# Kernel tuning notes

Hardware: AMD Instinct MI355X
Metric: run time of the kernel (lower is better)

The kernel has to match this reference:

```python
import jax, jax.numpy as jnp
import numpy as np

N = 8192
D_IN = 512
HID = 1024
EMB = 64
N_EFF = 2
N_CLASSES = 16
MARGIN = 0.01


def setup_inputs() -> dict:
    key = jax.random.key(0)
    ks = jax.random.split(key, 10)
    data = jax.random.normal(ks[0], (N, D_IN), dtype=jnp.float32)
    labels = jax.random.randint(ks[1], (N,), 0, N_CLASSES).astype(jnp.float32)
    x = jnp.concatenate([labels[:, None], data], axis=1)  # [N, 1+D_IN]

    def lin(k, fan_in, fan_out):
        return jax.random.normal(k, (fan_in, fan_out), dtype=jnp.float32) / np.sqrt(fan_in)

    return {
        "x": x,
        "W1": lin(ks[2], D_IN, HID), "b1": jnp.zeros((HID,), jnp.float32),
        "W2": lin(ks[3], HID, EMB), "b2": jnp.zeros((EMB,), jnp.float32),
        "W3": lin(ks[4], EMB, HID), "b3": jnp.zeros((HID,), jnp.float32),
        "W4": lin(ks[5], HID, D_IN), "b4": jnp.zeros((D_IN,), jnp.float32),
    }


def reference(x, W1, b1, W2, b2, W3, b3, W4, b4):
    labels = x[:, 0]
    data = x[:, 1:]

    # encoder / decoder (tanh MLP autoencoder)
    embedding = jnp.tanh(data @ W1 + b1) @ W2 + b2          # [N, EMB]
    decoded = jnp.tanh(embedding @ W3 + b3) @ W4 + b4       # [N, D_IN]

    conserved = embedding[:, N_EFF:]                        # [N, C]
    n_conserved = conserved.shape[1]

    # labels.expand + unique(return_inverse) on row-replicated labels is
    # equivalent to comparing the labels directly.
    lbl = labels.astype(jnp.int32)
    Y = lbl[:, None] != lbl[None, :]                        # [N, N] bool

    # D_mean[i,j] = mean_d (c_i - c_j)^2, via Gram-matrix algebra (one pass,
    # no [N,N,C] intermediate).
    sq = jnp.sum(conserved * conserved, axis=1)             # [N]
    gram = conserved @ conserved.T                          # [N, N]
    D_mean = jnp.maximum(sq[:, None] + sq[None, :] - 2.0 * gram, 0.0) / n_conserved

    Yf = Y.astype(D_mean.dtype)
    n_diff = jnp.sum(Yf)
    C_sim = jnp.sum(Yf * D_mean) / (n_diff + 1.0)
    C_diff = jnp.sum((1.0 - Yf) * jnp.maximum(0.0, MARGIN - D_mean)) / (
        (D_mean.shape[0] * D_mean.shape[1] - n_diff) + 1.0)

    return decoded, C_sim, C_diff
```

## Files before the change

### kernel.cpp

```cpp
#include <hip/hip_runtime.h>
#include <stdint.h>

#define NROWS 8192
#define DIN   512
#define HIDN  1024
#define EMBN  64
#define NCONS 62
#define NCLS  16
#define MARGINF 0.01f
#define NREP  16

typedef unsigned short u16;
typedef __attribute__((ext_vector_type(8))) short short8;
typedef __attribute__((ext_vector_type(4))) float floatx4;

__device__ __forceinline__ u16 f32_to_bf16(float f) {
  union { float f; uint32_t u; } x; x.f = f;
  uint32_t u = x.u;
  uint32_t r = (u + 0x7FFFu + ((u >> 16) & 1u)) >> 16;
  return (u16)r;
}

__device__ __forceinline__ float bf16_to_f32(u16 h) {
  union { uint32_t u; float f; } x; x.u = (uint32_t)h << 16;
  return x.f;
}

__device__ __forceinline__ float fast_tanh(float x) {
  float xc = fminf(fmaxf(x, -10.f), 10.f);
  float e = __expf(2.f * xc);
  return (e - 1.f) * __builtin_amdgcn_rcpf(e + 1.f);
}

__device__ __forceinline__ void pack_tile(const float* __restrict__ W,
                                          u16* __restrict__ Wp,
                                          int N, int KU, int t, int lane)
{
  const int r = lane >> 2, slot = lane & 3;
  const int c = slot ^ ((r >> 1) & 3);
  const int nt = t / KU, ku = t - nt * KU;
  const int n = nt * 16 + r;
  const int kb = ku * 32 + c * 8;
  short8 v;
#pragma unroll
  for (int j = 0; j < 8; ++j) v[j] = (short)f32_to_bf16(W[(size_t)(kb + j) * N + n]);
  *(short8*)(Wp + ((size_t)t * 64 + lane) * 8) = v;
}

__global__ __launch_bounds__(256)
void prep_all(const float* __restrict__ x,
              const float* __restrict__ W1, const float* __restrict__ W2,
              const float* __restrict__ W3, const float* __restrict__ W4,
              u16* __restrict__ A0p, u16* __restrict__ W1p,
              u16* __restrict__ W2p, u16* __restrict__ W3p,
              u16* __restrict__ W4p, float* __restrict__ slab,
              int* __restrict__ labels, int* __restrict__ hist32)
{
  __shared__ int hh[NCLS];
  const int b = blockIdx.x;
  const int tid = threadIdx.x;
  const int tl = tid >> 6, lane = tid & 63;
  if (b < 2048) {
    if (b < 32) {
      if (tid < NCLS) hh[tid] = 0;
      const int row = b * 256 + tid;
      const int lab = (int)x[(size_t)row * 513];
      labels[row] = lab;
      __syncthreads();
      atomicAdd(&hh[lab], 1);
      __syncthreads();
      if (tid < NCLS) hist32[b * NCLS + tid] = hh[tid];
    }
    const int t = b * 4 + tl;
    const int rt = t >> 4, ku = t & 15;
    const int r = lane & 15, q = lane >> 4;
    const float* src = x + (size_t)(rt * 16 + r) * 513 + 1 + ku * 32 + q * 8;
    short8 v;
#pragma unroll
    for (int j = 0; j < 8; ++j) v[j] = (short)f32_to_bf16(src[j]);
    *(short8*)(A0p + ((size_t)t * 64 + lane) * 8) = v;
  } else if (b < 2304) {
    pack_tile(W1, W1p, 1024, 16, (b - 2048) * 4 + tl, lane);
  } else if (b < 2336) {
    pack_tile(W2, W2p, 64, 32, (b - 2304) * 4 + tl, lane);
  } else if (b < 2368) {
    pack_tile(W3, W3p, 1024, 2, (b - 2336) * 4 + tl, lane);
  } else if (b < 2624) {
    pack_tile(W4, W4p, 512, 32, (b - 2368) * 4 + tl, lane);
  } else {
    float* dst = slab + (size_t)(b - 2624) * 4096;
    for (int i = tid; i < 4096; i += 256) dst[i] = 0.f;
  }
}

__global__ __launch_bounds__(512, 4)
void fused1234(const u16* __restrict__ A0p, const u16* __restrict__ W1p,
               const float* __restrict__ b1, const u16* __restrict__ W2p,
               const float* __restrict__ b2, const u16* __restrict__ W3p,
               const float* __restrict__ b3, const u16* __restrict__ W4p,
               const float* __restrict__ b4,
               const int* __restrict__ labels, const int* __restrict__ hist32,
               int* __restrict__ offs, int* __restrict__ counts,
               int* __restrict__ idx,
               u16* __restrict__ Ebf, float* __restrict__ sqrow,
               float* __restrict__ vsumR, float* __restrict__ SsumR,
               float* __restrict__ out)
{
  __shared__ u16 uni[16 * 1032];
  __shared__ u16 El[16 * 66];
  __shared__ float lv[NCLS][64];
  __shared__ float lsq[NCLS][64];
  __shared__ int colsum[NCLS], preblk[NCLS], scur[NCLS];

  const int tid = threadIdx.x;

  if (blockIdx.x < 16) {
    const int sb = blockIdx.x;
    if (tid < NCLS) {
      int s = 0, p = 0;
      for (int b2i = 0; b2i < 32; ++b2i) {
        const int h = hist32[b2i * NCLS + tid];
        s += h;
        if (b2i < sb * 2) p += h;
      }
      colsum[tid] = s;
      preblk[tid] = p;
    }
    __syncthreads();
    if (tid < NCLS) {
      int o = 0;
      for (int c = 0; c < tid; ++c) o += colsum[c];
      scur[tid] = o + preblk[tid];
      if (sb == 0) {
        counts[tid] = colsum[tid];
        offs[tid] = o;
        if (tid == NCLS - 1) offs[NCLS] = o + colsum[NCLS - 1];
      }
    }
    __syncthreads();
    {
      const int row = sb * 512 + tid;
      const int p = atomicAdd(&scur[labels[row]], 1);
      idx[p] = row;
    }
    return;
  }

  const int bx = blockIdx.x - 16;
  const int m0 = bx * 16;
  const int rep = blockIdx.x & (NREP - 1);
  const int w = tid >> 6, lane = tid & 63;
  const int quad = lane >> 4, l15 = lane & 15;
  const int lamb = l15 * 4 + (quad ^ ((l15 >> 1) & 3));

  for (int i = tid; i < NCLS * 64; i += 512) {
    ((float*)lv)[i] = 0.f; ((float*)lsq)[i] = 0.f;
  }

  u16* Hc = uni;
  float* Epart = (float*)uni;
  u16* Tl = uni;

  const u16* Wbase = W1p + (size_t)(w * 8) * 16 * 512 + lamb * 8;
  const u16* Abase = A0p + (size_t)(bx * 16) * 512 + lane * 8;

  floatx4 acc1[8];
#pragma unroll
  for (int jj = 0; jj < 8; ++jj) acc1[jj] = (floatx4){0.f, 0.f, 0.f, 0.f};

  short8 bfb[2][8];
  short8 afb[2];
  afb[0] = *(const short8*)(Abase);
#pragma unroll
  for (int jj = 0; jj < 8; ++jj)
    bfb[0][jj] = *(const short8*)(Wbase + (size_t)(jj * 16) * 512);

#pragma unroll
  for (int s = 0; s < 16; ++s) {
    const int cur = s & 1, nxt = cur ^ 1;
    if (s < 15) {
      afb[nxt] = *(const short8*)(Abase + (size_t)(s + 1) * 512);
#pragma unroll
      for (int jj = 0; jj < 8; ++jj)
        bfb[nxt][jj] = *(const short8*)(Wbase + (size_t)(jj * 16 + s + 1) * 512);
    }
#pragma unroll
    for (int jj = 0; jj < 8; ++jj)
      acc1[jj] = __builtin_amdgcn_mfma_f32_16x16x32_bf16(afb[cur], bfb[cur][jj], acc1[jj], 0, 0, 0);
  }

#pragma unroll
  for (int jj = 0; jj < 8; ++jj) {
    const int col = w * 128 + jj * 16 + l15;
    const float bv = b1[col];
#pragma unroll
    for (int r = 0; r < 4; ++r)
      Hc[(quad * 4 + r) * 1032 + col] = f32_to_bf16(fast_tanh(acc1[jj][r] + bv));
  }
  __syncthreads();

  floatx4 acc2[4];
#pragma unroll
  for (int nt = 0; nt < 4; ++nt) acc2[nt] = (floatx4){0.f, 0.f, 0.f, 0.f};

#pragma unroll
  for (int kk = 0; kk < 4; ++kk) {
    const int ku = w * 4 + kk;
    const short8 af = *(const short8*)(Hc + l15 * 1032 + ku * 32 + quad * 8);
#pragma unroll
    for (int nt = 0; nt < 4; ++nt) {
      const short8 bf = *(const short8*)(W2p + (size_t)(nt * 32 + ku) * 512 + lamb * 8);
      acc2[nt] = __builtin_amdgcn_mfma_f32_16x16x32_bf16(af, bf, acc2[nt], 0, 0, 0);
    }
  }
  __syncthreads();

#pragma unroll
  for (int nt = 0; nt < 4; ++nt)
#pragma unroll
    for (int r = 0; r < 4; ++r)
      Epart[((size_t)w * 16 + quad * 4 + r) * 64 + nt * 16 + l15] = acc2[nt][r];
  __syncthreads();

  {
    const float bv2 = b2[lane];
    for (int r = 0; r < 2; ++r) {
      const int row = w * 2 + r;
      const int grow = m0 + row;
      const int c = labels[grow];
      float acc = bv2;
#pragma unroll
      for (int p = 0; p < 8; ++p)
        acc += Epart[((size_t)p * 16 + row) * 64 + lane];
      const u16 h = f32_to_bf16(acc);
      Ebf[(size_t)grow * 64 + lane] = h;
      El[row * 66 + lane] = h;
      float v = bf16_to_f32(h);
      if (lane < 2) v = 0.f;
      const float v2 = v * v;
      atomicAdd(&lv[c][lane], v);
      atomicAdd(&lsq[c][lane], v2);
      float s = v2;
      for (int o = 32; o > 0; o >>= 1) s += __shfl_xor(s, o);
      if (lane == 0) sqrow[grow] = s;
    }
  }
  __syncthreads();

  for (int i = tid; i < NCLS * 64; i += 512) {
    const int c = i >> 6, k = i & 63;
    if (k >= 2) atomicAdd(&vsumR[rep * (NCLS * NCONS) + c * NCONS + k - 2], lv[c][k]);
  }
  if (tid < NCLS) {
    float s = 0.f;
    for (int k = 0; k < 64; ++k) s += lsq[tid][k];
    atomicAdd(&SsumR[rep * NCLS + tid], s);
  }

  floatx4 acc3[8];
#pragma unroll
  for (int jj = 0; jj < 8; ++jj) acc3[jj] = (floatx4){0.f, 0.f, 0.f, 0.f};

#pragma unroll
  for (int kk = 0; kk < 2; ++kk) {
    const short8 af = *(const short8*)(El + l15 * 66 + kk * 32 + quad * 8);
#pragma unroll
    for (int jj = 0; jj < 8; ++jj) {
      const int nt = w * 8 + jj;
      const short8 bf = *(const short8*)(W3p + (size_t)(nt * 2 + kk) * 512 + lamb * 8);
      acc3[jj] = __builtin_amdgcn_mfma_f32_16x16x32_bf16(af, bf, acc3[jj], 0, 0, 0);
    }
  }
#pragma unroll
  for (int jj = 0; jj < 8; ++jj) {
    const int col = w * 128 + jj * 16 + l15;
    const float bv3 = b3[col];
#pragma unroll
    for (int r = 0; r < 4; ++r)
      Tl[(quad * 4 + r) * 1032 + col] = f32_to_bf16(fast_tanh(acc3[jj][r] + bv3));
  }
  __syncthreads();

  const u16* W4base = W4p + (size_t)(w * 4) * 32 * 512 + lamb * 8;

  floatx4 acc4[4];
#pragma unroll
  for (int nt = 0; nt < 4; ++nt) acc4[nt] = (floatx4){0.f, 0.f, 0.f, 0.f};

  short8 b4b[2][4];
  short8 a4b[2];
  a4b[0] = *(const short8*)(Tl + l15 * 1032 + quad * 8);
#pragma unroll
  for (int nt = 0; nt < 4; ++nt)
    b4b[0][nt] = *(const short8*)(W4base + (size_t)(nt * 32) * 512);

#pragma unroll
  for (int ku = 0; ku < 32; ++ku) {
    const int cur = ku & 1, nxt = cur ^ 1;
    if (ku < 31) {
      a4b[nxt] = *(const short8*)(Tl + l15 * 1032 + (ku + 1) * 32 + quad * 8);
#pragma unroll
      for (int nt = 0; nt < 4; ++nt)
        b4b[nxt][nt] = *(const short8*)(W4base + (size_t)(nt * 32 + ku + 1) * 512);
    }
#pragma unroll
    for (int nt = 0; nt < 4; ++nt)
      acc4[nt] = __builtin_amdgcn_mfma_f32_16x16x32_bf16(a4b[cur], b4b[cur][nt], acc4[nt], 0, 0, 0);
  }

#pragma unroll
  for (int nt = 0; nt < 4; ++nt) {
    const int col = w * 64 + nt * 16 + l15;
    const float bv4 = b4[col];
#pragma unroll
    for (int r = 0; r < 4; ++r) {
      const int row = m0 + quad * 4 + r;
      out[(size_t)row * 512 + col] = acc4[nt][r] + bv4;
    }
  }
}

__global__ __launch_bounds__(256)
void pairwise_mfma(const u16* __restrict__ Ebf, const float* __restrict__ sqrow,
                   const int* __restrict__ idx, const int* __restrict__ offs,
                   float* __restrict__ pair_sum)
{
  const int q = blockIdx.x;
  const int cls = q / 21;
  int p = q - cls * 21, ti = 0, cnt = 6;
  while (p >= cnt) { p -= cnt; ++ti; --cnt; }
  const int tj = ti + p;

  const int start = offs[cls];
  const int n = offs[cls + 1] - start;
  if (ti * 128 >= n || tj * 128 >= n) return;

  constexpr int LDA = 66;
  __shared__ u16 Li[128 * LDA];
  __shared__ u16 Lj[128 * LDA];
  __shared__ float sqI[128], sqJ[128];
  __shared__ float red4[4];

  const int tid = threadIdx.x, wave = tid >> 6, lane = tid & 63;
  const int quad = lane >> 4, l15 = lane & 15;

  for (int e = tid; e < 2048; e += 256) {
    const int t = e >> 10;
    const int row = (e >> 3) & 127;
    const int ch = e & 7;
    const int g = (t ? tj : ti) * 128 + row;
    short8 v = (short8)0;
    if (g < n) {
      v = *(const short8*)(Ebf + (size_t)idx[start + g] * EMBN + ch * 8);
      if (ch == 0) { v[0] = 0; v[1] = 0; }
    }
    *(short8*)((t ? Lj : Li) + row * LDA + ch * 8) = v;
  }
  {
    const int t = tid >> 7, row = tid & 127;
    const int g = (t ? tj : ti) * 128 + row;
    (t ? sqJ : sqI)[row] = (g < n) ? sqrow[idx[start + g]] : 0.f;
  }
  __syncthreads();

  const int wm = wave >> 1, wn = wave & 1;

  floatx4 acc[4][4];
#pragma unroll
  for (int i = 0; i < 4; ++i)
#pragma unroll
    for (int j = 0; j < 4; ++j) acc[i][j] = (floatx4){0.f, 0.f, 0.f, 0.f};

#pragma unroll
  for (int ks = 0; ks < 2; ++ks) {
    short8 af[4], bf[4];
#pragma unroll
    for (int i = 0; i < 4; ++i)
      af[i] = *(const short8*)(Li + (wm * 64 + i * 16 + l15) * LDA + ks * 32 + quad * 8);
#pragma unroll
    for (int j = 0; j < 4; ++j)
      bf[j] = *(const short8*)(Lj + (wn * 64 + j * 16 + l15) * LDA + ks * 32 + quad * 8);
#pragma unroll
    for (int i = 0; i < 4; ++i)
#pragma unroll
      for (int j = 0; j < 4; ++j)
        acc[i][j] = __builtin_amdgcn_mfma_f32_16x16x32_bf16(af[i], bf[j], acc[i][j], 0, 0, 0);
  }

  float local = 0.f;
#pragma unroll
  for (int i = 0; i < 4; ++i)
#pragma unroll
    for (int j = 0; j < 4; ++j)
#pragma unroll
      for (int r = 0; r < 4; ++r) {
        const int row = wm * 64 + i * 16 + quad * 4 + r;
        const int col = wn * 64 + j * 16 + l15;
        const int gi = ti * 128 + row, gj = tj * 128 + col;
        if (gi < n && gj < n && gi != gj) {
          const float D = (sqI[row] + sqJ[col] - 2.f * acc[i][j][r]) * (1.f / 62.f);
          local += fmaxf(0.f, MARGINF - D);
        }
      }
  if (ti < tj) local *= 2.f;

  for (int o = 32; o > 0; o >>= 1) local += __shfl_xor(local, o);
  if (lane == 0) red4[wave] = local;
  __syncthreads();
  if (tid == 0)
    atomicAdd(pair_sum, red4[0] + red4[1] + red4[2] + red4[3]);
}

__device__ __forceinline__ double block_reduce_d(double v, double* red, int tid) {
  red[tid] = v;
  __syncthreads();
  for (int st = 128; st > 0; st >>= 1) {
    if (tid < st) red[tid] += red[tid + st];
    __syncthreads();
  }
  const double r = red[0];
  __syncthreads();
  return r;
}

__global__ __launch_bounds__(256)
void finalize(const float* __restrict__ vsumR, const float* __restrict__ SsumR,
              const int* __restrict__ counts, const float* __restrict__ pair_sum,
              float* __restrict__ out2)
{
  const int tid = threadIdx.x;
  __shared__ double red[256];
  __shared__ float vtot[NCLS * NCONS];

  for (int i = tid; i < NCLS * NCONS; i += 256) {
    float s = 0.f;
    for (int r = 0; r < NREP; ++r) s += vsumR[r * (NCLS * NCONS) + i];
    vtot[i] = s;
  }
  __syncthreads();

  double v = 0.0;
  if (tid < NCLS) {
    float Sc = 0.f;
    for (int r = 0; r < NREP; ++r) Sc += SsumR[r * NCLS + tid];
    v = (double)Sc * (double)(NROWS - counts[tid]);
  }
  const double t1 = block_reduce_d(v, red, tid);

  v = 0.0;
  if (tid < NCLS) { const double nc = (double)counts[tid]; v = nc * nc; }
  const double n_same = block_reduce_d(v, red, tid);

  v = 0.0;
  for (int i = tid; i < NCLS * NCONS; i += 256) { const double w = vtot[i]; v += w * w; }
  const double t2 = block_reduce_d(v, red, tid);

  v = 0.0;
  if (tid < NCONS) {
    double Vk = 0.0;
    for (int c = 0; c < NCLS; ++c) Vk += (double)vtot[c * NCONS + tid];
    v = Vk * Vk;
  }
  const double t3 = block_reduce_d(v, red, tid);

  if (tid == 0) {
    const double n_diff = (double)NROWS * (double)NROWS - n_same;
    const double sim = 2.0 * t1 - 2.0 * (t3 - t2);
    const double C_sim = sim / 62.0 / (n_diff + 1.0);
    const double C_diff = ((double)pair_sum[0] + (double)NROWS * (double)MARGINF)
                          / (n_same + 1.0);
    out2[0] = (float)C_sim;
    out2[1] = (float)C_diff;
  }
}

extern "C" void kernel_launch(void* const* d_in, const int* in_sizes, int n_in,
                              void* d_out, int out_size, void* d_ws, size_t ws_size,
                              hipStream_t stream)
{
  const float* x  = (const float*)d_in[0];
  const float* W1 = (const float*)d_in[1];
  const float* b1 = (const float*)d_in[2];
  const float* W2 = (const float*)d_in[3];
  const float* b2 = (const float*)d_in[4];
  const float* W3 = (const float*)d_in[5];
  const float* b3 = (const float*)d_in[6];
  const float* W4 = (const float*)d_in[7];
  const float* b4 = (const float*)d_in[8];
  float* out = (float*)d_out;

  char* ws = (char*)d_ws;
  const size_t KB = 1024, MB = 1ull << 20;
  u16* A0p    = (u16*)(ws + 0);
  u16* W1p    = (u16*)(ws + 8 * MB);
  u16* W2p    = (u16*)(ws + 9 * MB);
  u16* W3p    = (u16*)(ws + 9 * MB + 128 * KB);
  u16* W4p    = (u16*)(ws + 9 * MB + 256 * KB);
  u16* Ebf    = (u16*)(ws + 18 * MB + 256 * KB);
  int* labels = (int*)(ws + 19 * MB + 256 * KB);
  int* idx    = (int*)(ws + 19 * MB + 288 * KB);
  float* sqrow = (float*)(ws + 19 * MB + 320 * KB);
  int* hist32 = (int*)(ws + 19 * MB + 352 * KB);
  float* slab = (float*)(ws + 19 * MB + 384 * KB);
  int*   counts  = (int*)slab;
  int*   offs    = counts + 16;
  float* psum    = slab + 64;
  float* SsumR   = slab + 128;
  float* vsumR   = slab + 512;
  (void)in_sizes; (void)n_in; (void)out_size; (void)ws_size;

  prep_all<<<dim3(2630), dim3(256), 0, stream>>>(x, W1, W2, W3, W4,
                                                 A0p, W1p, W2p, W3p, W4p,
                                                 slab, labels, hist32);
  fused1234<<<dim3(528), dim3(512), 0, stream>>>(A0p, W1p, b1, W2p, b2, W3p, b3,
                                                 W4p, b4,
                                                 labels, hist32, offs, counts, idx,
                                                 Ebf, sqrow, vsumR, SsumR, out);
  pairwise_mfma<<<dim3(336), dim3(256), 0, stream>>>(Ebf, sqrow, idx, offs, psum);
  finalize<<<dim3(1), dim3(256), 0, stream>>>(vsumR, SsumR, counts, psum,
                                              out + (size_t)NROWS * DIN);
}
```

Before: 159.9 us.

## Process 32 rows per block in fused MLP to reuse weight fragments

Each block of the fused encoder/decoder kernel now handles two 16-row tiles instead of one, so every weight fragment loaded from global memory feeds two MFMAs. This halves total weight traffic across the four GEMM stages and cuts the grid from 512 compute blocks to 256. In exchange, per-thread accumulator registers and LDS usage double, occupancy is lowered via launch bounds, and with 256 blocks the GPU may be underfilled.

```diff
diff --git a/kernel.cpp b/kernel.cpp
--- a/kernel.cpp
+++ b/kernel.cpp
@@ -93,7 +93,7 @@
   }
 }
 
-__global__ __launch_bounds__(512, 4)
+__global__ __launch_bounds__(512, 2)
 void fused1234(const u16* __restrict__ A0p, const u16* __restrict__ W1p,
                const float* __restrict__ b1, const u16* __restrict__ W2p,
                const float* __restrict__ b2, const u16* __restrict__ W3p,
@@ -106,8 +106,8 @@
                float* __restrict__ vsumR, float* __restrict__ SsumR,
                float* __restrict__ out)
 {
-  __shared__ u16 uni[16 * 1032];
-  __shared__ u16 El[16 * 66];
+  __shared__ u16 uni[32 * 1032];
+  __shared__ u16 El[32 * 66];
   __shared__ float lv[NCLS][64];
   __shared__ float lsq[NCLS][64];
   __shared__ int colsum[NCLS], preblk[NCLS], scur[NCLS];
@@ -147,7 +147,7 @@
   }
 
   const int bx = blockIdx.x - 16;
-  const int m0 = bx * 16;
+  const int m0 = bx * 32;
   const int rep = blockIdx.x & (NREP - 1);
   const int w = tid >> 6, lane = tid & 63;
   const int quad = lane >> 4, l15 = lane & 15;
@@ -162,15 +162,19 @@
   u16* Tl = uni;
 
   const u16* Wbase = W1p + (size_t)(w * 8) * 16 * 512 + lamb * 8;
-  const u16* Abase = A0p + (size_t)(bx * 16) * 512 + lane * 8;
-
-  floatx4 acc1[8];
-#pragma unroll
-  for (int jj = 0; jj < 8; ++jj) acc1[jj] = (floatx4){0.f, 0.f, 0.f, 0.f};
+  const u16* Abase0 = A0p + (size_t)((2 * bx + 0) * 16) * 512 + lane * 8;
+  const u16* Abase1 = A0p + (size_t)((2 * bx + 1) * 16) * 512 + lane * 8;
+
+  floatx4 acc1[2][8];
+#pragma unroll
+  for (int i = 0; i < 2; ++i)
+#pragma unroll
+    for (int jj = 0; jj < 8; ++jj) acc1[i][jj] = (floatx4){0.f, 0.f, 0.f, 0.f};
 
   short8 bfb[2][8];
-  short8 afb[2];
-  afb[0] = *(const short8*)(Abase);
+  short8 afb[2][2];
+  afb[0][0] = *(const short8*)(Abase0);
+  afb[0][1] = *(const short8*)(Abase1);
 #pragma unroll
   for (int jj = 0; jj < 8; ++jj)
     bfb[0][jj] = *(const short8*)(Wbase + (size_t)(jj * 16) * 512);
@@ -179,14 +183,17 @@
   for (int s = 0; s < 16; ++s) {
     const int cur = s & 1, nxt = cur ^ 1;
     if (s < 15) {
-      afb[nxt] = *(const short8*)(Abase + (size_t)(s + 1) * 512);
+      afb[nxt][0] = *(const short8*)(Abase0 + (size_t)(s + 1) * 512);
+      afb[nxt][1] = *(const short8*)(Abase1 + (size_t)(s + 1) * 512);
 #pragma unroll
       for (int jj = 0; jj < 8; ++jj)
         bfb[nxt][jj] = *(const short8*)(Wbase + (size_t)(jj * 16 + s + 1) * 512);
     }
 #pragma unroll
     for (int jj = 0; jj < 8; ++jj)
-      acc1[jj] = __builtin_amdgcn_mfma_f32_16x16x32_bf16(afb[cur], bfb[cur][jj], acc1[jj], 0, 0, 0);
+#pragma unroll
+      for (int i = 0; i < 2; ++i)
+        acc1[i][jj] = __builtin_amdgcn_mfma_f32_16x16x32_bf16(afb[cur][i], bfb[cur][jj], acc1[i][jj], 0, 0, 0);
   }
 
 #pragma unroll
@@ -194,44 +201,55 @@
     const int col = w * 128 + jj * 16 + l15;
     const float bv = b1[col];
 #pragma unroll
-    for (int r = 0; r < 4; ++r)
-      Hc[(quad * 4 + r) * 1032 + col] = f32_to_bf16(fast_tanh(acc1[jj][r] + bv));
-  }
-  __syncthreads();
-
-  floatx4 acc2[4];
-#pragma unroll
-  for (int nt = 0; nt < 4; ++nt) acc2[nt] = (floatx4){0.f, 0.f, 0.f, 0.f};
+    for (int i = 0; i < 2; ++i)
+#pragma unroll
+      for (int r = 0; r < 4; ++r)
+        Hc[(i * 16 + quad * 4 + r) * 1032 + col] = f32_to_bf16(fast_tanh(acc1[i][jj][r] + bv));
+  }
+  __syncthreads();
+
+  floatx4 acc2[2][4];
+#pragma unroll
+  for (int i = 0; i < 2; ++i)
+#pragma unroll
+    for (int nt = 0; nt < 4; ++nt) acc2[i][nt] = (floatx4){0.f, 0.f, 0.f, 0.f};
 
 #pragma unroll
   for (int kk = 0; kk < 4; ++kk) {
     const int ku = w * 4 + kk;
-    const short8 af = *(const short8*)(Hc + l15 * 1032 + ku * 32 + quad * 8);
+    short8 af[2];
+#pragma unroll
+    for (int i = 0; i < 2; ++i)
+      af[i] = *(const short8*)(Hc + (i * 16 + l15) * 1032 + ku * 32 + quad * 8);
 #pragma unroll
     for (int nt = 0; nt < 4; ++nt) {
       const short8 bf = *(const short8*)(W2p + (size_t)(nt * 32 + ku) * 512 + lamb * 8);
-      acc2[nt] = __builtin_amdgcn_mfma_f32_16x16x32_bf16(af, bf, acc2[nt], 0, 0, 0);
-    }
-  }
-  __syncthreads();
-
-#pragma unroll
-  for (int nt = 0; nt < 4; ++nt)
-#pragma unroll
-    for (int r = 0; r < 4; ++r)
-      Epart[((size_t)w * 16 + quad * 4 + r) * 64 + nt * 16 + l15] = acc2[nt][r];
+#pragma unroll
+      for (int i = 0; i < 2; ++i)
+        acc2[i][nt] = __builtin_amdgcn_mfma_f32_16x16x32_bf16(af[i], bf, acc2[i][nt], 0, 0, 0);
+    }
+  }
+  __syncthreads();
+
+#pragma unroll
+  for (int i = 0; i < 2; ++i)
+#pragma unroll
+    for (int nt = 0; nt < 4; ++nt)
+#pragma unroll
+      for (int r = 0; r < 4; ++r)
+        Epart[((size_t)w * 32 + i * 16 + quad * 4 + r) * 64 + nt * 16 + l15] = acc2[i][nt][r];
   __syncthreads();
 
   {
     const float bv2 = b2[lane];
-    for (int r = 0; r < 2; ++r) {
-      const int row = w * 2 + r;
+    for (int r = 0; r < 4; ++r) {
+      const int row = w * 4 + r;
       const int grow = m0 + row;
       const int c = labels[grow];
       float acc = bv2;
 #pragma unroll
       for (int p = 0; p < 8; ++p)
-        acc += Epart[((size_t)p * 16 + row) * 64 + lane];
+        acc += Epart[((size_t)p * 32 + row) * 64 + lane];
       const u16 h = f32_to_bf16(acc);
       Ebf[(size_t)grow * 64 + lane] = h;
       El[row * 66 + lane] = h;
@@ -257,18 +275,25 @@
     atomicAdd(&SsumR[rep * NCLS + tid], s);
   }
 
-  floatx4 acc3[8];
-#pragma unroll
-  for (int jj = 0; jj < 8; ++jj) acc3[jj] = (floatx4){0.f, 0.f, 0.f, 0.f};
+  floatx4 acc3[2][8];
+#pragma unroll
+  for (int i = 0; i < 2; ++i)
+#pragma unroll
+    for (int jj = 0; jj < 8; ++jj) acc3[i][jj] = (floatx4){0.f, 0.f, 0.f, 0.f};
 
 #pragma unroll
   for (int kk = 0; kk < 2; ++kk) {
-    const short8 af = *(const short8*)(El + l15 * 66 + kk * 32 + quad * 8);
+    short8 af[2];
+#pragma unroll
+    for (int i = 0; i < 2; ++i)
+      af[i] = *(const short8*)(El + (i * 16 + l15) * 66 + kk * 32 + quad * 8);
 #pragma unroll
     for (int jj = 0; jj < 8; ++jj) {
       const int nt = w * 8 + jj;
       const short8 bf = *(const short8*)(W3p + (size_t)(nt * 2 + kk) * 512 + lamb * 8);
-      acc3[jj] = __builtin_amdgcn_mfma_f32_16x16x32_bf16(af, bf, acc3[jj], 0, 0, 0);
+#pragma unroll
+      for (int i = 0; i < 2; ++i)
+        acc3[i][jj] = __builtin_amdgcn_mfma_f32_16x16x32_bf16(af[i], bf, acc3[i][jj], 0, 0, 0);
     }
   }
 #pragma unroll
@@ -276,20 +301,25 @@
     const int col = w * 128 + jj * 16 + l15;
     const float bv3 = b3[col];
 #pragma unroll
-    for (int r = 0; r < 4; ++r)
-      Tl[(quad * 4 + r) * 1032 + col] = f32_to_bf16(fast_tanh(acc3[jj][r] + bv3));
+    for (int i = 0; i < 2; ++i)
+#pragma unroll
+      for (int r = 0; r < 4; ++r)
+        Tl[(i * 16 + quad * 4 + r) * 1032 + col] = f32_to_bf16(fast_tanh(acc3[i][jj][r] + bv3));
   }
   __syncthreads();
 
   const u16* W4base = W4p + (size_t)(w * 4) * 32 * 512 + lamb * 8;
 
-  floatx4 acc4[4];
-#pragma unroll
-  for (int nt = 0; nt < 4; ++nt) acc4[nt] = (floatx4){0.f, 0.f, 0.f, 0.f};
+  floatx4 acc4[2][4];
+#pragma unroll
+  for (int i = 0; i < 2; ++i)
+#pragma unroll
+    for (int nt = 0; nt < 4; ++nt) acc4[i][nt] = (floatx4){0.f, 0.f, 0.f, 0.f};
 
   short8 b4b[2][4];
-  short8 a4b[2];
-  a4b[0] = *(const short8*)(Tl + l15 * 1032 + quad * 8);
+  short8 a4b[2][2];
+  a4b[0][0] = *(const short8*)(Tl + (0 * 16 + l15) * 1032 + quad * 8);
+  a4b[0][1] = *(const short8*)(Tl + (1 * 16 + l15) * 1032 + quad * 8);
 #pragma unroll
   for (int nt = 0; nt < 4; ++nt)
     b4b[0][nt] = *(const short8*)(W4base + (size_t)(nt * 32) * 512);
@@ -298,14 +328,17 @@
   for (int ku = 0; ku < 32; ++ku) {
     const int cur = ku & 1, nxt = cur ^ 1;
     if (ku < 31) {
-      a4b[nxt] = *(const short8*)(Tl + l15 * 1032 + (ku + 1) * 32 + quad * 8);
+      a4b[nxt][0] = *(const short8*)(Tl + (0 * 16 + l15) * 1032 + (ku + 1) * 32 + quad * 8);
+      a4b[nxt][1] = *(const short8*)(Tl + (1 * 16 + l15) * 1032 + (ku + 1) * 32 + quad * 8);
 #pragma unroll
       for (int nt = 0; nt < 4; ++nt)
         b4b[nxt][nt] = *(const short8*)(W4base + (size_t)(nt * 32 + ku + 1) * 512);
     }
 #pragma unroll
     for (int nt = 0; nt < 4; ++nt)
-      acc4[nt] = __builtin_amdgcn_mfma_f32_16x16x32_bf16(a4b[cur], b4b[cur][nt], acc4[nt], 0, 0, 0);
+#pragma unroll
+      for (int i = 0; i < 2; ++i)
+        acc4[i][nt] = __builtin_amdgcn_mfma_f32_16x16x32_bf16(a4b[cur][i], b4b[cur][nt], acc4[i][nt], 0, 0, 0);
   }
 
 #pragma unroll
@@ -313,10 +346,12 @@
     const int col = w * 64 + nt * 16 + l15;
     const float bv4 = b4[col];
 #pragma unroll
-    for (int r = 0; r < 4; ++r) {
-      const int row = m0 + quad * 4 + r;
-      out[(size_t)row * 512 + col] = acc4[nt][r] + bv4;
-    }
+    for (int i = 0; i < 2; ++i)
+#pragma unroll
+      for (int r = 0; r < 4; ++r) {
+        const int row = m0 + i * 16 + quad * 4 + r;
+        out[(size_t)row * 512 + col] = acc4[i][nt][r] + bv4;
+      }
   }
 }
 
@@ -512,7 +547,7 @@
   prep_all<<<dim3(2630), dim3(256), 0, stream>>>(x, W1, W2, W3, W4,
                                                  A0p, W1p, W2p, W3p, W4p,
                                                  slab, labels, hist32);
-  fused1234<<<dim3(528), dim3(512), 0, stream>>>(A0p, W1p, b1, W2p, b2, W3p, b3,
+  fused1234<<<dim3(272), dim3(512), 0, stream>>>(A0p, W1p, b1, W2p, b2, W3p, b3,
                                                  W4p, b4,
                                                  labels, hist32, offs, counts, idx,
                                                  Ebf, sqrow, vsumR, SsumR, out);
```

After: 171.7 us. +7.3%, slower.

## Split decoder's final GEMM into separate kernel co-scheduled with pairwise loss blocks

Applied to the files above, without the earlier changes.

The W4 decoder GEMM moves out of the fused MLP kernel. The tanh hidden activations T are now written to a bf16 global buffer, and a new 'tail' kernel runs the W4 GEMM with 32x256 tiles per 256-thread block. The same launch also carries the pairwise contrastive-loss blocks, so both kinds of work overlap. The goal is shorter per-block serial work in the fused kernel and a merged pairwise launch, at the cost of an extra 16MB round trip of T through global memory and one extra kernel boundary.

```diff
diff --git a/kernel.cpp b/kernel.cpp
--- a/kernel.cpp
+++ b/kernel.cpp
@@ -94,17 +94,16 @@
 }
 
 __global__ __launch_bounds__(512, 4)
-void fused1234(const u16* __restrict__ A0p, const u16* __restrict__ W1p,
-               const float* __restrict__ b1, const u16* __restrict__ W2p,
-               const float* __restrict__ b2, const u16* __restrict__ W3p,
-               const float* __restrict__ b3, const u16* __restrict__ W4p,
-               const float* __restrict__ b4,
-               const int* __restrict__ labels, const int* __restrict__ hist32,
-               int* __restrict__ offs, int* __restrict__ counts,
-               int* __restrict__ idx,
-               u16* __restrict__ Ebf, float* __restrict__ sqrow,
-               float* __restrict__ vsumR, float* __restrict__ SsumR,
-               float* __restrict__ out)
+void fused123(const u16* __restrict__ A0p, const u16* __restrict__ W1p,
+              const float* __restrict__ b1, const u16* __restrict__ W2p,
+              const float* __restrict__ b2, const u16* __restrict__ W3p,
+              const float* __restrict__ b3,
+              const int* __restrict__ labels, const int* __restrict__ hist32,
+              int* __restrict__ offs, int* __restrict__ counts,
+              int* __restrict__ idx,
+              u16* __restrict__ Ebf, float* __restrict__ sqrow,
+              float* __restrict__ vsumR, float* __restrict__ SsumR,
+              u16* __restrict__ T)
 {
   __shared__ u16 uni[16 * 1032];
   __shared__ u16 El[16 * 66];
@@ -159,7 +158,6 @@
 
   u16* Hc = uni;
   float* Epart = (float*)uni;
-  u16* Tl = uni;
 
   const u16* Wbase = W1p + (size_t)(w * 8) * 16 * 512 + lamb * 8;
   const u16* Abase = A0p + (size_t)(bx * 16) * 512 + lane * 8;
@@ -277,64 +275,18 @@
     const float bv3 = b3[col];
 #pragma unroll
     for (int r = 0; r < 4; ++r)
-      Tl[(quad * 4 + r) * 1032 + col] = f32_to_bf16(fast_tanh(acc3[jj][r] + bv3));
-  }
-  __syncthreads();
-
-  const u16* W4base = W4p + (size_t)(w * 4) * 32 * 512 + lamb * 8;
-
-  floatx4 acc4[4];
-#pragma unroll
-  for (int nt = 0; nt < 4; ++nt) acc4[nt] = (floatx4){0.f, 0.f, 0.f, 0.f};
-
-  short8 b4b[2][4];
-  short8 a4b[2];
-  a4b[0] = *(const short8*)(Tl + l15 * 1032 + quad * 8);
-#pragma unroll
-  for (int nt = 0; nt < 4; ++nt)
-    b4b[0][nt] = *(const short8*)(W4base + (size_t)(nt * 32) * 512);
-
-#pragma unroll
-  for (int ku = 0; ku < 32; ++ku) {
-    const int cur = ku & 1, nxt = cur ^ 1;
-    if (ku < 31) {
-      a4b[nxt] = *(const short8*)(Tl + l15 * 1032 + (ku + 1) * 32 + quad * 8);
-#pragma unroll
-      for (int nt = 0; nt < 4; ++nt)
-        b4b[nxt][nt] = *(const short8*)(W4base + (size_t)(nt * 32 + ku + 1) * 512);
-    }
-#pragma unroll
-    for (int nt = 0; nt < 4; ++nt)
-      acc4[nt] = __builtin_amdgcn_mfma_f32_16x16x32_bf16(a4b[cur], b4b[cur][nt], acc4[nt], 0, 0, 0);
-  }
-
-#pragma unroll
-  for (int nt = 0; nt < 4; ++nt) {
-    const int col = w * 64 + nt * 16 + l15;
-    const float bv4 = b4[col];
-#pragma unroll
-    for (int r = 0; r < 4; ++r) {
-      const int row = m0 + quad * 4 + r;
-      out[(size_t)row * 512 + col] = acc4[nt][r] + bv4;
-    }
-  }
-}
-
-__global__ __launch_bounds__(256)
-void pairwise_mfma(const u16* __restrict__ Ebf, const float* __restrict__ sqrow,
-                   const int* __restrict__ idx, const int* __restrict__ offs,
-                   float* __restrict__ pair_sum)
+      T[(size_t)(m0 + quad * 4 + r) * 1024 + col] =
+          f32_to_bf16(fast_tanh(acc3[jj][r] + bv3));
+  }
+}
+
+__global__ __launch_bounds__(256, 4)
+void tail(const u16* __restrict__ T, const u16* __restrict__ W4p,
+          const float* __restrict__ b4, float* __restrict__ out,
+          const u16* __restrict__ Ebf, const float* __restrict__ sqrow,
+          const int* __restrict__ idx, const int* __restrict__ offs,
+          float* __restrict__ pair_sum)
 {
-  const int q = blockIdx.x;
-  const int cls = q / 21;
-  int p = q - cls * 21, ti = 0, cnt = 6;
-  while (p >= cnt) { p -= cnt; ++ti; --cnt; }
-  const int tj = ti + p;
-
-  const int start = offs[cls];
-  const int n = offs[cls + 1] - start;
-  if (ti * 128 >= n || tj * 128 >= n) return;
-
   constexpr int LDA = 66;
   __shared__ u16 Li[128 * LDA];
   __shared__ u16 Lj[128 * LDA];
@@ -343,6 +295,72 @@
 
   const int tid = threadIdx.x, wave = tid >> 6, lane = tid & 63;
   const int quad = lane >> 4, l15 = lane & 15;
+
+  if (blockIdx.x < 512) {
+    const int lin = blockIdx.x;
+    const int m0 = (lin & 255) * 32;
+    const int c0 = (lin >> 8) * 256;
+    const int w = wave;
+    const int lamb = l15 * 4 + (quad ^ ((l15 >> 1) & 3));
+
+    const u16* W4base = W4p + (size_t)((c0 >> 4) + w * 4) * 32 * 512 + lamb * 8;
+    const u16* Tb0 = T + (size_t)(m0 + 0 * 16 + l15) * 1024 + quad * 8;
+    const u16* Tb1 = T + (size_t)(m0 + 1 * 16 + l15) * 1024 + quad * 8;
+
+    floatx4 acc4[2][4];
+#pragma unroll
+    for (int i = 0; i < 2; ++i)
+#pragma unroll
+      for (int nt = 0; nt < 4; ++nt) acc4[i][nt] = (floatx4){0.f, 0.f, 0.f, 0.f};
+
+    short8 a4b[2][2], b4b[2][4];
+    a4b[0][0] = *(const short8*)(Tb0);
+    a4b[0][1] = *(const short8*)(Tb1);
+#pragma unroll
+    for (int nt = 0; nt < 4; ++nt)
+      b4b[0][nt] = *(const short8*)(W4base + (size_t)(nt * 32) * 512);
+
+#pragma unroll
+    for (int ku = 0; ku < 32; ++ku) {
+      const int cur = ku & 1, nxt = cur ^ 1;
+      if (ku < 31) {
+        a4b[nxt][0] = *(const short8*)(Tb0 + (size_t)(ku + 1) * 32);
+        a4b[nxt][1] = *(const short8*)(Tb1 + (size_t)(ku + 1) * 32);
+#pragma unroll
+        for (int nt = 0; nt < 4; ++nt)
+          b4b[nxt][nt] = *(const short8*)(W4base + (size_t)(nt * 32 + ku + 1) * 512);
+      }
+#pragma unroll
+      for (int nt = 0; nt < 4; ++nt)
+#pragma unroll
+        for (int i = 0; i < 2; ++i)
+          acc4[i][nt] = __builtin_amdgcn_mfma_f32_16x16x32_bf16(a4b[cur][i], b4b[cur][nt], acc4[i][nt], 0, 0, 0);
+    }
+
+#pragma unroll
+    for (int nt = 0; nt < 4; ++nt) {
+      const int col = c0 + w * 64 + nt * 16 + l15;
+      const float bv4 = b4[col];
+#pragma unroll
+      for (int i = 0; i < 2; ++i)
+#pragma unroll
+        for (int r = 0; r < 4; ++r) {
+          const int row = m0 + i * 16 + quad * 4 + r;
+          out[(size_t)row * 512 + col] = acc4[i][nt][r] + bv4;
+        }
+    }
+    return;
+  }
+
+  const int q = blockIdx.x - 512;
+  const int cls = q / 21;
+  int p = q - cls * 21, ti = 0, cnt = 6;
+  while (p >= cnt) { p -= cnt; ++ti; --cnt; }
+  const int tj = ti + p;
+
+  const int start = offs[cls];
+  const int n = offs[cls + 1] - start;
+  if (ti * 128 >= n || tj * 128 >= n) return;
 
   for (int e = tid; e < 2048; e += 256) {
     const int t = e >> 10;
@@ -507,16 +525,17 @@
   float* psum    = slab + 64;
   float* SsumR   = slab + 128;
   float* vsumR   = slab + 512;
+  u16* T      = (u16*)(ws + 20 * MB);
   (void)in_sizes; (void)n_in; (void)out_size; (void)ws_size;
 
   prep_all<<<dim3(2630), dim3(256), 0, stream>>>(x, W1, W2, W3, W4,
                                                  A0p, W1p, W2p, W3p, W4p,
                                                  slab, labels, hist32);
-  fused1234<<<dim3(528), dim3(512), 0, stream>>>(A0p, W1p, b1, W2p, b2, W3p, b3,
-                                                 W4p, b4,
-                                                 labels, hist32, offs, counts, idx,
-                                                 Ebf, sqrow, vsumR, SsumR, out);
-  pairwise_mfma<<<dim3(336), dim3(256), 0, stream>>>(Ebf, sqrow, idx, offs, psum);
+  fused123<<<dim3(528), dim3(512), 0, stream>>>(A0p, W1p, b1, W2p, b2, W3p, b3,
+                                                labels, hist32, offs, counts, idx,
+                                                Ebf, sqrow, vsumR, SsumR, T);
+  tail<<<dim3(848), dim3(256), 0, stream>>>(T, W4p, b4, out,
+                                            Ebf, sqrow, idx, offs, psum);
   finalize<<<dim3(1), dim3(256), 0, stream>>>(vsumR, SsumR, counts, psum,
                                               out + (size_t)NROWS * DIN);
 }
```

Measured after the change: 161.2 us. No clear change (+0.8%).
